# Optimization experiments

Hardware: AMD Instinct MI355X
Metric: run time of the kernel (lower is better)

The kernel has to match this reference:

```python
import jax, jax.numpy as jnp
import numpy as np

N = 131072
CODE_DIM = 64
HIDDEN = 128
DT_MAX = 0.125
N_STEPS = 8  # = ceil(max|t1-t2| / DT_MAX); extra steps are exact no-ops since dt=0 for finished rows


def setup_inputs() -> dict:
    key = jax.random.key(0)
    ks = jax.random.split(key, 8)
    deform_code = jax.random.normal(ks[0], (N, CODE_DIM), dtype=jnp.float32)
    pos_init = jax.random.normal(ks[1], (N, 3), dtype=jnp.float32)
    t1 = jax.random.uniform(ks[2], (N, 1), dtype=jnp.float32)
    t2 = jnp.zeros((N, 1), dtype=jnp.float32)
    # vel_net MLP params: concat(code, xyzt)[68] -> 128 -> 128 -> 3, tanh activations
    s1 = 1.0 / np.sqrt(CODE_DIM + 4)
    s2 = 1.0 / np.sqrt(HIDDEN)
    W1 = jax.random.normal(ks[3], (CODE_DIM + 4, HIDDEN), dtype=jnp.float32) * s1
    b1 = jnp.zeros((HIDDEN,), dtype=jnp.float32)
    W2 = jax.random.normal(ks[4], (HIDDEN, HIDDEN), dtype=jnp.float32) * s2
    b2 = jnp.zeros((HIDDEN,), dtype=jnp.float32)
    W3 = jax.random.normal(ks[5], (HIDDEN, 3), dtype=jnp.float32) * s2
    b3 = jnp.zeros((3,), dtype=jnp.float32)
    return {"deform_code": deform_code, "pos_init": pos_init, "t1": t1, "t2": t2,
            "W1": W1, "b1": b1, "W2": W2, "b2": b2, "W3": W3, "b3": b3}


def reference(deform_code, pos_init, t1, t2, W1, b1, W2, b2, W3, b3):
    def get_vel(code, xyzt):  # works for single sample or batch
        x = jnp.concatenate([code, xyzt], axis=-1)
        h = jnp.tanh(x @ W1 + b1)
        h = jnp.tanh(h @ W2 + b2)
        return h @ W3 + b3

    def u_func(code, xyzt):  # per-sample, for jacobian wrt xyzt (argnums=1)
        u = get_vel(code, xyzt)
        return u, u

    jac_fn = jax.vmap(jax.jacrev(u_func, argnums=1, has_aux=True))  # [N,3,4] jac, [N,3] vel

    n = pos_init.shape[0]
    deform0 = jnp.broadcast_to(jnp.eye(3, dtype=pos_init.dtype), (n, 3, 3))

    def step(state, _):
        xyz, t_curr, offset, deform = state
        # dt == 0 exactly for finished rows -> all updates below are no-ops (matches masked in-place updates)
        dt = jnp.sign(offset) * jnp.minimum(jnp.abs(offset), DT_MAX)  # [N,1]
        v0 = get_vel(deform_code, jnp.concatenate([xyz, t_curr], axis=-1))
        p_mid = xyz - 0.5 * dt * v0
        t_mid = t_curr - 0.5 * dt
        jac_v, velocity = jac_fn(deform_code, jnp.concatenate([p_mid, t_mid], axis=-1))
        drotdt = jnp.einsum('noi,nij->noj', jac_v[:, :3, :3], deform)
        deform = deform - dt[..., None] * drotdt
        xyz = xyz - dt * velocity
        return (xyz, t_curr - dt, offset - dt, deform), None

    state0 = (pos_init, t1, t1 - t2, deform0)
    (xyz, _, _, deform), _ = jax.lax.scan(step, state0, None, length=N_STEPS)
    return xyz, deform
```

## Files before the change

kernel.cpp:

```cpp
#include <hip/hip_runtime.h>
#include <hip/hip_bf16.h>

#define H 128
#define NSTEPS 8
#define DT_MAXF 0.125f
#define WAVES 4
#define PPW 16
#define PPB (WAVES*PPW)

typedef __attribute__((ext_vector_type(8))) short short8;
typedef __attribute__((ext_vector_type(4))) float floatx4;
typedef __attribute__((ext_vector_type(2))) float f32x2;

__device__ __forceinline__ f32x2 sp2(float v) { return (f32x2){v, v}; }
__device__ __forceinline__ f32x2 fma2(f32x2 a, f32x2 b, f32x2 c) {
    return __builtin_elementwise_fma(a, b, c);
}
__device__ __forceinline__ f32x2 tanh2(f32x2 x) {
    f32x2 y = x * 2.8853900817779268f;
    f32x2 e; e[0] = __builtin_amdgcn_exp2f(y[0]); e[1] = __builtin_amdgcn_exp2f(y[1]);
    f32x2 ep = e + 1.0f;
    float rt = __builtin_amdgcn_rcpf(ep[0] * ep[1]);
    f32x2 eps = __builtin_shufflevector(ep, ep, 1, 0);
    f32x2 r = eps * sp2(rt);
    return fma2(sp2(-2.0f), r, sp2(1.0f));
}
__device__ __forceinline__ unsigned f2bf(float x) {
    unsigned u = __float_as_uint(x);
    return (u + 0x7FFFu + ((u >> 16) & 1u)) >> 16;
}
__device__ __forceinline__ unsigned pk2(float a, float b) {
    union { __hip_bfloat162 h; unsigned u; } U;
    U.h = __float22bfloat162_rn(make_float2(a, b));
    return U.u;
}
__device__ __forceinline__ unsigned pkv(f32x2 v) { return pk2(v[0], v[1]); }
__device__ __forceinline__ short8 mk8(unsigned a, unsigned b, unsigned c, unsigned d) {
    union { unsigned u[4]; short8 s; } U;
    U.u[0] = a; U.u[1] = b; U.u[2] = c; U.u[3] = d; return U.s;
}
__device__ __forceinline__ short8 xyzt_frag(float x, float y, float z, float t, int q) {
    unsigned hx = f2bf(x), hy = f2bf(y), hz = f2bf(z), ht = f2bf(t);
    float lx = x - __uint_as_float(hx << 16);
    float ly = y - __uint_as_float(hy << 16);
    float lz = z - __uint_as_float(hz << 16);
    float lt = t - __uint_as_float(ht << 16);
    unsigned w0 = hx | (hy << 16), w1 = hz | (ht << 16);
    unsigned w2 = pk2(lx, ly),     w3 = pk2(lz, lt);
    union { unsigned u[4]; short8 s; } F;
    F.u[0] = (q < 2)  ? w0 : 0u;
    F.u[1] = (q < 2)  ? w1 : 0u;
    F.u[2] = (q == 0) ? w2 : 0u;
    F.u[3] = (q == 0) ? w3 : 0u;
    return F.s;
}

__device__ __forceinline__ int step_bucket(float t1v, float t2v) {
    float off = fabsf(t1v - t2v);
    int b = (int)ceilf(off * 8.0f);
    return min(max(b, 0), 8);
}
__global__ void prep_zero(unsigned* cnt) {
    if (threadIdx.x < 18) cnt[threadIdx.x] = 0u;
}
__global__ void prep_hist(const float* __restrict__ t1g, const float* __restrict__ t2g,
                          unsigned* cnt, int N) {
    __shared__ unsigned h[9];
    if (threadIdx.x < 9) h[threadIdx.x] = 0u;
    __syncthreads();
    int i = blockIdx.x * 256 + threadIdx.x;
    if (i < N) atomicAdd(&h[step_bucket(t1g[i], t2g[i])], 1u);
    __syncthreads();
    if (threadIdx.x < 9 && h[threadIdx.x]) atomicAdd(&cnt[threadIdx.x], h[threadIdx.x]);
}
__global__ void prep_prefix(unsigned* cnt) {
    if (threadIdx.x == 0) {
        unsigned run = 0;
        for (int b = 0; b < 9; ++b) { unsigned c = cnt[b]; cnt[9 + b] = run; run += c; }
    }
}
__global__ void prep_scatter(const float* __restrict__ t1g, const float* __restrict__ t2g,
                             unsigned* cnt, int* __restrict__ perm, int N) {
    __shared__ unsigned h[9];
    __shared__ unsigned base[9];
    if (threadIdx.x < 9) h[threadIdx.x] = 0u;
    __syncthreads();
    int i = blockIdx.x * 256 + threadIdx.x;
    int b = 0; unsigned r = 0;
    if (i < N) {
        b = step_bucket(t1g[i], t2g[i]);
        r = atomicAdd(&h[b], 1u);
    }
    __syncthreads();
    if (threadIdx.x < 9 && h[threadIdx.x])
        base[threadIdx.x] = atomicAdd(&cnt[9 + threadIdx.x], h[threadIdx.x]);
    __syncthreads();
    if (i < N) perm[base[b] + r] = i;
}

__global__ __launch_bounds__(256, 2)
void velwarp(const float* __restrict__ code, const float* __restrict__ pos,
             const float* __restrict__ t1g, const float* __restrict__ t2g,
             const float* __restrict__ W1, const float* __restrict__ b1,
             const float* __restrict__ W2, const float* __restrict__ b2,
             const float* __restrict__ W3, const float* __restrict__ b3,
             float* __restrict__ out, const int* __restrict__ perm, int N)
{
    __shared__ __align__(16) uint4 WbufU[2048];
    __shared__ __align__(16) uint4 W1AU[8*64];
    __shared__ __align__(16) uint4 W3AU[4*64];
    __shared__ __align__(16) floatx4 WdX4[32];
    __shared__ __align__(16) floatx4 WdY4[32];
    __shared__ __align__(16) floatx4 WdZ4[32];
    __shared__ __align__(16) floatx4 b2C4[32];

    const int tid = threadIdx.x;
    const int L   = tid & 63;
    const int m   = L & 15;
    const int q   = L >> 4;
    const int pb  = blockIdx.x * PPB + (tid >> 6) * PPW;
    const int p   = perm ? perm[pb + m] : (pb + m);

    {
        const float4* s4 = (const float4*)W1;
        float4* d4 = (float4*)WbufU;
        #pragma unroll 4
        for (int i = tid; i < (64*H)/4; i += 256) d4[i] = s4[i];
    }
    for (int e = tid; e < 512; e += 256) {
        int t = e >> 6, l = e & 63;
        int u = t*16 + (l & 15), qq = l >> 4;
        unsigned hb[4], lb[4];
        #pragma unroll
        for (int c = 0; c < 4; ++c) {
            float wv = W1[(64 + c)*H + u];
            unsigned hh = f2bf(wv);
            float wl = wv - __uint_as_float(hh << 16);
            hb[c] = hh; lb[c] = f2bf(wl);
        }
        unsigned hi01 = hb[0] | (hb[1] << 16), hi23 = hb[2] | (hb[3] << 16);
        unsigned lo01 = lb[0] | (lb[1] << 16), lo23 = lb[2] | (lb[3] << 16);
        uint4 o;
        if (qq == 0)      o = make_uint4(hi01, hi23, hi01, hi23);
        else if (qq == 1) o = make_uint4(lo01, lo23, 0u, 0u);
        else              o = make_uint4(0u, 0u, 0u, 0u);
        W1AU[e] = o;
    }
    for (int e = tid; e < 256; e += 256) {
        int s = e >> 6, l = e & 63;
        int a = l & 15, qq = l >> 4;
        uint4 o = make_uint4(0u, 0u, 0u, 0u);
        if (a < 3) {
            int u0 = s*32 + qq*4, u1 = u0 + 16;
            o.x = f2bf(W3[(u0+0)*3+a]) | (f2bf(W3[(u0+1)*3+a]) << 16);
            o.y = f2bf(W3[(u0+2)*3+a]) | (f2bf(W3[(u0+3)*3+a]) << 16);
            o.z = f2bf(W3[(u1+0)*3+a]) | (f2bf(W3[(u1+1)*3+a]) << 16);
            o.w = f2bf(W3[(u1+2)*3+a]) | (f2bf(W3[(u1+3)*3+a]) << 16);
        }
        W3AU[e] = o;
    }
    if (tid < 32) {
        WdX4[tid] = ((const floatx4*)(W1 + (size_t)64*H))[tid];
        WdY4[tid] = ((const floatx4*)(W1 + (size_t)65*H))[tid];
        WdZ4[tid] = ((const floatx4*)(W1 + (size_t)66*H))[tid];
        b2C4[tid] = ((const floatx4*)b2)[tid];
    }
    __syncthreads();

    floatx4 base1C[8];
    {
        #pragma unroll
        for (int t = 0; t < 8; ++t) base1C[t] = *(const floatx4*)&b1[t*16 + q*4];
        const float* Ws = (const float*)WbufU;
        const float* crow = code + (size_t)p * 64;
        for (int i = 0; i < 64; ++i) {
            f32x2 c = sp2(crow[i]);
            #pragma unroll
            for (int t = 0; t < 8; ++t) {
                floatx4 wq = *(const floatx4*)&Ws[i*H + t*16 + q*4];
                base1C[t].xy = fma2(c, wq.xy, base1C[t].xy);
                base1C[t].zw = fma2(c, wq.zw, base1C[t].zw);
            }
        }
    }
    __syncthreads();

    for (int ch = tid; ch < 2048; ch += 256) {
        int ln = ch & 63, ts = ch >> 6;
        int s = ts & 3, t = ts >> 2;
        int qq = ln >> 4, n = t*16 + (ln & 15);
        int u0 = s*32 + qq*4, u1 = u0 + 16;
        unsigned w0 = f2bf(W2[(u0+0)*H+n]) | (f2bf(W2[(u0+1)*H+n]) << 16);
        unsigned w1 = f2bf(W2[(u0+2)*H+n]) | (f2bf(W2[(u0+3)*H+n]) << 16);
        unsigned w2 = f2bf(W2[(u1+0)*H+n]) | (f2bf(W2[(u1+1)*H+n]) << 16);
        unsigned w3v = f2bf(W2[(u1+2)*H+n]) | (f2bf(W2[(u1+3)*H+n]) << 16);
        WbufU[ch] = make_uint4(w0, w1, w2, w3v);
    }

    float px_ = pos[p*3+0], py_ = pos[p*3+1], pz_ = pos[p*3+2];
    float tc_ = t1g[p];
    float off_ = tc_ - t2g[p];
    f32x2 Dp[3]; float Ds[3];
    Dp[0] = (f32x2){1.f, 0.f}; Ds[0] = 0.f;
    Dp[1] = (f32x2){0.f, 1.f}; Ds[1] = 0.f;
    Dp[2] = (f32x2){0.f, 0.f}; Ds[2] = 1.f;
    const float b30 = b3[0], b31 = b3[1], b32 = b3[2];
    __syncthreads();

    const short8* Bf   = (const short8*)WbufU;
    const short8* W1Af = (const short8*)W1AU;
    const short8* W3Af = (const short8*)W3AU;
    const floatx4 Z4 = {0.f, 0.f, 0.f, 0.f};

    for (int step = 0; step < NSTEPS; ++step) {
        if (!__any(off_ != 0.0f)) break;

        float vAx, vAy, vAz;
        {
            short8 xf = xyzt_frag(px_, py_, pz_, tc_, q);
            floatx4 z[8];
            #pragma unroll
            for (int t = 0; t < 8; ++t)
                z[t] = __builtin_amdgcn_mfma_f32_16x16x32_bf16(W1Af[t*64 + L], xf, base1C[t], 0, 0, 0);
            short8 fh[4];
            #pragma unroll
            for (int s = 0; s < 4; ++s) {
                f32x2 a0 = tanh2(z[2*s].xy),   a1 = tanh2(z[2*s].zw);
                f32x2 c0 = tanh2(z[2*s+1].xy), c1 = tanh2(z[2*s+1].zw);
                fh[s] = mk8(pkv(a0), pkv(a1), pkv(c0), pkv(c1));
            }
            __builtin_amdgcn_sched_barrier(0);
            floatx4 vacc = Z4;
            #pragma unroll
            for (int qi = 0; qi < 4; ++qi) {
                const int T0 = 2*qi, T1 = 2*qi + 1;
                floatx4 acc0 = __builtin_amdgcn_mfma_f32_16x16x32_bf16(
                    Bf[(T0*4 + 0)*64 + L], fh[0], b2C4[T0*4 + q], 0, 0, 0);
                floatx4 acc1 = __builtin_amdgcn_mfma_f32_16x16x32_bf16(
                    Bf[(T1*4 + 0)*64 + L], fh[0], b2C4[T1*4 + q], 0, 0, 0);
                #pragma unroll
                for (int s = 1; s < 4; ++s) {
                    acc0 = __builtin_amdgcn_mfma_f32_16x16x32_bf16(Bf[(T0*4 + s)*64 + L], fh[s], acc0, 0, 0, 0);
                    acc1 = __builtin_amdgcn_mfma_f32_16x16x32_bf16(Bf[(T1*4 + s)*64 + L], fh[s], acc1, 0, 0, 0);
                }
                f32x2 e00 = tanh2(acc0.xy), e01 = tanh2(acc0.zw);
                f32x2 e10 = tanh2(acc1.xy), e11 = tanh2(acc1.zw);
                short8 ef = mk8(pkv(e00), pkv(e01), pkv(e10), pkv(e11));
                vacc = __builtin_amdgcn_mfma_f32_16x16x32_bf16(W3Af[qi*64 + L], ef, vacc, 0, 0, 0);
                __builtin_amdgcn_sched_barrier(0);
            }
            vAx = __shfl(vacc[0], m, 64);
            vAy = __shfl(vacc[1], m, 64);
            vAz = __shfl(vacc[2], m, 64);
        }

        float dt_ = copysignf(fminf(fabsf(off_), DT_MAXF), off_);
        float hd = 0.5f * dt_;
        float mx = px_ - hd*(vAx + b30);
        float my = py_ - hd*(vAy + b31);
        float mz = pz_ - hd*(vAz + b32);
        float tm = tc_ - hd;

        float vx, vy, vz;
        floatx4 V = Z4, J0 = Z4, J1 = Z4, J2 = Z4;
        {
            short8 xf = xyzt_frag(mx, my, mz, tm, q);
            floatx4 z[8];
            #pragma unroll
            for (int t = 0; t < 8; ++t)
                z[t] = __builtin_amdgcn_mfma_f32_16x16x32_bf16(W1Af[t*64 + L], xf, base1C[t], 0, 0, 0);
            short8 fh[4], fd0[4], fd1[4], fd2[4];
            #pragma unroll
            for (int s = 0; s < 4; ++s) {
                unsigned uh[4], u0[4], u1[4], u2[4];
                #pragma unroll
                for (int hf = 0; hf < 2; ++hf) {
                    int t = 2*s + hf;
                    f32x2 h0 = tanh2(z[t].xy), h1 = tanh2(z[t].zw);
                    f32x2 s0 = fma2(-h0, h0, sp2(1.0f));
                    f32x2 s1 = fma2(-h1, h1, sp2(1.0f));
                    floatx4 wx = WdX4[t*4 + q], wy = WdY4[t*4 + q], wz = WdZ4[t*4 + q];
                    uh[2*hf+0] = pkv(h0);         uh[2*hf+1] = pkv(h1);
                    u0[2*hf+0] = pkv(s0 * wx.xy); u0[2*hf+1] = pkv(s1 * wx.zw);
                    u1[2*hf+0] = pkv(s0 * wy.xy); u1[2*hf+1] = pkv(s1 * wy.zw);
                    u2[2*hf+0] = pkv(s0 * wz.xy); u2[2*hf+1] = pkv(s1 * wz.zw);
                }
                fh[s]  = mk8(uh[0], uh[1], uh[2], uh[3]);
                fd0[s] = mk8(u0[0], u0[1], u0[2], u0[3]);
                fd1[s] = mk8(u1[0], u1[1], u1[2], u1[3]);
                fd2[s] = mk8(u2[0], u2[1], u2[2], u2[3]);
            }
            __builtin_amdgcn_sched_barrier(0);
            #pragma unroll
            for (int qi = 0; qi < 4; ++qi) {
                const int T0 = 2*qi, T1 = 2*qi + 1;
                floatx4 aH0, aH1, aD00, aD01, aD10, aD11, aD20, aD21;
                {
                    short8 A0 = Bf[(T0*4 + 0)*64 + L];
                    short8 A1 = Bf[(T1*4 + 0)*64 + L];
                    aH0  = __builtin_amdgcn_mfma_f32_16x16x32_bf16(A0, fh[0],  b2C4[T0*4 + q], 0, 0, 0);
                    aH1  = __builtin_amdgcn_mfma_f32_16x16x32_bf16(A1, fh[0],  b2C4[T1*4 + q], 0, 0, 0);
                    aD00 = __builtin_amdgcn_mfma_f32_16x16x32_bf16(A0, fd0[0], Z4, 0, 0, 0);
                    aD01 = __builtin_amdgcn_mfma_f32_16x16x32_bf16(A1, fd0[0], Z4, 0, 0, 0);
                    aD10 = __builtin_amdgcn_mfma_f32_16x16x32_bf16(A0, fd1[0], Z4, 0, 0, 0);
                    aD11 = __builtin_amdgcn_mfma_f32_16x16x32_bf16(A1, fd1[0], Z4, 0, 0, 0);
                    aD20 = __builtin_amdgcn_mfma_f32_16x16x32_bf16(A0, fd2[0], Z4, 0, 0, 0);
                    aD21 = __builtin_amdgcn_mfma_f32_16x16x32_bf16(A1, fd2[0], Z4, 0, 0, 0);
                }
                #pragma unroll
                for (int s = 1; s < 4; ++s) {
                    short8 A0 = Bf[(T0*4 + s)*64 + L];
                    short8 A1 = Bf[(T1*4 + s)*64 + L];
                    aH0  = __builtin_amdgcn_mfma_f32_16x16x32_bf16(A0, fh[s],  aH0,  0, 0, 0);
                    aH1  = __builtin_amdgcn_mfma_f32_16x16x32_bf16(A1, fh[s],  aH1,  0, 0, 0);
                    aD00 = __builtin_amdgcn_mfma_f32_16x16x32_bf16(A0, fd0[s], aD00, 0, 0, 0);
                    aD01 = __builtin_amdgcn_mfma_f32_16x16x32_bf16(A1, fd0[s], aD01, 0, 0, 0);
                    aD10 = __builtin_amdgcn_mfma_f32_16x16x32_bf16(A0, fd1[s], aD10, 0, 0, 0);
                    aD11 = __builtin_amdgcn_mfma_f32_16x16x32_bf16(A1, fd1[s], aD11, 0, 0, 0);
                    aD20 = __builtin_amdgcn_mfma_f32_16x16x32_bf16(A0, fd2[s], aD20, 0, 0, 0);
                    aD21 = __builtin_amdgcn_mfma_f32_16x16x32_bf16(A1, fd2[s], aD21, 0, 0, 0);
                }
                f32x2 h0 = tanh2(aH0.xy), h1 = tanh2(aH0.zw);
                f32x2 h2v = tanh2(aH1.xy), h3 = tanh2(aH1.zw);
                f32x2 s0 = fma2(-h0, h0, sp2(1.0f));
                f32x2 s1 = fma2(-h1, h1, sp2(1.0f));
                f32x2 s2v = fma2(-h2v, h2v, sp2(1.0f));
                f32x2 s3 = fma2(-h3, h3, sp2(1.0f));
                short8 eh = mk8(pkv(h0), pkv(h1), pkv(h2v), pkv(h3));
                short8 e0 = mk8(pkv(s0*aD00.xy), pkv(s1*aD00.zw), pkv(s2v*aD01.xy), pkv(s3*aD01.zw));
                short8 e1 = mk8(pkv(s0*aD10.xy), pkv(s1*aD10.zw), pkv(s2v*aD11.xy), pkv(s3*aD11.zw));
                short8 e2 = mk8(pkv(s0*aD20.xy), pkv(s1*aD20.zw), pkv(s2v*aD21.xy), pkv(s3*aD21.zw));
                const short8 WA = W3Af[qi*64 + L];
                V  = __builtin_amdgcn_mfma_f32_16x16x32_bf16(WA, eh, V,  0, 0, 0);
                J0 = __builtin_amdgcn_mfma_f32_16x16x32_bf16(WA, e0, J0, 0, 0, 0);
                J1 = __builtin_amdgcn_mfma_f32_16x16x32_bf16(WA, e1, J1, 0, 0, 0);
                J2 = __builtin_amdgcn_mfma_f32_16x16x32_bf16(WA, e2, J2, 0, 0, 0);
                __builtin_amdgcn_sched_barrier(0);
            }
            vx = __shfl(V[0], m, 64) + b30;
            vy = __shfl(V[1], m, 64) + b31;
            vz = __shfl(V[2], m, 64) + b32;
        }

        {
            f32x2 ndp[3]; float nds[3];
            #pragma unroll
            for (int o = 0; o < 3; ++o) {
                f32x2 tp = J0[o] * Dp[0];
                tp = fma2(sp2(J1[o]), Dp[1], tp);
                tp = fma2(sp2(J2[o]), Dp[2], tp);
                ndp[o] = fma2(sp2(-dt_), tp, Dp[o]);
                float ts = J0[o]*Ds[0];
                ts = fmaf(J1[o], Ds[1], ts);
                ts = fmaf(J2[o], Ds[2], ts);
                nds[o] = fmaf(-dt_, ts, Ds[o]);
            }
            #pragma unroll
            for (int o = 0; o < 3; ++o) { Dp[o] = ndp[o]; Ds[o] = nds[o]; }
        }
        px_ = fmaf(-dt_, vx, px_);
        py_ = fmaf(-dt_, vy, py_);
        pz_ = fmaf(-dt_, vz, pz_);
        tc_  -= dt_;
        off_ -= dt_;
    }

    if (q == 0) {
        out[p*3+0] = px_; out[p*3+1] = py_; out[p*3+2] = pz_;
        float* o9 = out + (size_t)N*3 + (size_t)p*9;
        #pragma unroll
        for (int o = 0; o < 3; ++o) {
            o9[o*3+0] = Dp[o][0];
            o9[o*3+1] = Dp[o][1];
            o9[o*3+2] = Ds[o];
        }
    }
}

extern "C" void kernel_launch(void* const* d_in, const int* in_sizes, int n_in,
                              void* d_out, int out_size, void* d_ws, size_t ws_size,
                              hipStream_t stream) {
    const float* code = (const float*)d_in[0];
    const float* pos  = (const float*)d_in[1];
    const float* t1   = (const float*)d_in[2];
    const float* t2   = (const float*)d_in[3];
    const float* W1   = (const float*)d_in[4];
    const float* b1   = (const float*)d_in[5];
    const float* W2   = (const float*)d_in[6];
    const float* b2   = (const float*)d_in[7];
    const float* W3   = (const float*)d_in[8];
    const float* b3   = (const float*)d_in[9];
    float* out = (float*)d_out;
    const int N = in_sizes[1] / 3;
    const int blocks = N / PPB;

    const size_t need = 128 + (size_t)N * sizeof(int);
    int* perm = nullptr;
    if (d_ws && ws_size >= need) {
        unsigned* cnt = (unsigned*)d_ws;
        perm = (int*)((char*)d_ws + 128);
        const int pblocks = (N + 255) / 256;
        prep_zero<<<1, 64, 0, stream>>>(cnt);
        prep_hist<<<pblocks, 256, 0, stream>>>(t1, t2, cnt, N);
        prep_prefix<<<1, 64, 0, stream>>>(cnt);
        prep_scatter<<<pblocks, 256, 0, stream>>>(t1, t2, cnt, perm, N);
    }
    velwarp<<<blocks, 256, 0, stream>>>(code, pos, t1, t2, W1, b1, W2, b2, W3, b3, out, perm, N);
}
```

Before: 302.3 us.

## Compute code projection with split-bf16 MFMA, reverse bucket order, memset counters

```diff
diff --git a/kernel.cpp b/kernel.cpp
--- a/kernel.cpp
+++ b/kernel.cpp
@@ -60,9 +60,6 @@
     int b = (int)ceilf(off * 8.0f);
     return min(max(b, 0), 8);
 }
-__global__ void prep_zero(unsigned* cnt) {
-    if (threadIdx.x < 18) cnt[threadIdx.x] = 0u;
-}
 __global__ void prep_hist(const float* __restrict__ t1g, const float* __restrict__ t2g,
                           unsigned* cnt, int N) {
     __shared__ unsigned h[9];
@@ -76,7 +73,7 @@
 __global__ void prep_prefix(unsigned* cnt) {
     if (threadIdx.x == 0) {
         unsigned run = 0;
-        for (int b = 0; b < 9; ++b) { unsigned c = cnt[b]; cnt[9 + b] = run; run += c; }
+        for (int b = 8; b >= 0; --b) { unsigned c = cnt[b]; cnt[9 + b] = run; run += c; }
     }
 }
 __global__ void prep_scatter(const float* __restrict__ t1g, const float* __restrict__ t2g,
@@ -121,11 +118,24 @@
     const int pb  = blockIdx.x * PPB + (tid >> 6) * PPW;
     const int p   = perm ? perm[pb + m] : (pb + m);
 
-    {
-        const float4* s4 = (const float4*)W1;
-        float4* d4 = (float4*)WbufU;
-        #pragma unroll 4
-        for (int i = tid; i < (64*H)/4; i += 256) d4[i] = s4[i];
+    for (int e = tid; e < 1024; e += 256) {
+        int t = e >> 7, rem = e & 127;
+        int c = rem >> 6, l = rem & 63;
+        int qq = l >> 4, mm = l & 15;
+        int u = t*16 + mm;
+        int g0 = c*32 + qq*4, g1 = g0 + 16;
+        unsigned hh[8]; float lo[8];
+        #pragma unroll
+        for (int j = 0; j < 4; ++j) {
+            float w0 = W1[(g0+j)*H + u];
+            float w1 = W1[(g1+j)*H + u];
+            hh[j]   = f2bf(w0); lo[j]   = w0 - __uint_as_float(hh[j]   << 16);
+            hh[4+j] = f2bf(w1); lo[4+j] = w1 - __uint_as_float(hh[4+j] << 16);
+        }
+        WbufU[((t*2+c)*2+0)*64 + l] = make_uint4(hh[0]|(hh[1]<<16), hh[2]|(hh[3]<<16),
+                                                 hh[4]|(hh[5]<<16), hh[6]|(hh[7]<<16));
+        WbufU[((t*2+c)*2+1)*64 + l] = make_uint4(pk2(lo[0],lo[1]), pk2(lo[2],lo[3]),
+                                                 pk2(lo[4],lo[5]), pk2(lo[6],lo[7]));
     }
     for (int e = tid; e < 512; e += 256) {
         int t = e >> 6, l = e & 63;
@@ -169,18 +179,36 @@
 
     floatx4 base1C[8];
     {
+        const float4* crow4 = (const float4*)(code + (size_t)p * 64);
+        short8 Bh[2], Bl[2];
         #pragma unroll
-        for (int t = 0; t < 8; ++t) base1C[t] = *(const floatx4*)&b1[t*16 + q*4];
-        const float* Ws = (const float*)WbufU;
-        const float* crow = code + (size_t)p * 64;
-        for (int i = 0; i < 64; ++i) {
-            f32x2 c = sp2(crow[i]);
-            #pragma unroll
-            for (int t = 0; t < 8; ++t) {
-                floatx4 wq = *(const floatx4*)&Ws[i*H + t*16 + q*4];
-                base1C[t].xy = fma2(c, wq.xy, base1C[t].xy);
-                base1C[t].zw = fma2(c, wq.zw, base1C[t].zw);
-            }
+        for (int c = 0; c < 2; ++c) {
+            float4 a = crow4[c*8 + q];
+            float4 b = crow4[c*8 + 4 + q];
+            unsigned h0 = f2bf(a.x), h1 = f2bf(a.y), h2 = f2bf(a.z), h3 = f2bf(a.w);
+            unsigned g0 = f2bf(b.x), g1 = f2bf(b.y), g2 = f2bf(b.z), g3 = f2bf(b.w);
+            float l0 = a.x - __uint_as_float(h0<<16), l1 = a.y - __uint_as_float(h1<<16);
+            float l2 = a.z - __uint_as_float(h2<<16), l3 = a.w - __uint_as_float(h3<<16);
+            float m0 = b.x - __uint_as_float(g0<<16), m1 = b.y - __uint_as_float(g1<<16);
+            float m2 = b.z - __uint_as_float(g2<<16), m3 = b.w - __uint_as_float(g3<<16);
+            Bh[c] = mk8(h0|(h1<<16), h2|(h3<<16), g0|(g1<<16), g2|(g3<<16));
+            Bl[c] = mk8(pk2(l0,l1), pk2(l2,l3), pk2(m0,m1), pk2(m2,m3));
+        }
+        const short8* Wb = (const short8*)WbufU;
+        #pragma unroll
+        for (int t = 0; t < 8; ++t) {
+            floatx4 z = *(const floatx4*)&b1[t*16 + q*4];
+            short8 Wh0 = Wb[((t*2+0)*2+0)*64 + L];
+            short8 Wh1 = Wb[((t*2+1)*2+0)*64 + L];
+            short8 Wl0 = Wb[((t*2+0)*2+1)*64 + L];
+            short8 Wl1 = Wb[((t*2+1)*2+1)*64 + L];
+            z = __builtin_amdgcn_mfma_f32_16x16x32_bf16(Wh0, Bh[0], z, 0, 0, 0);
+            z = __builtin_amdgcn_mfma_f32_16x16x32_bf16(Wh1, Bh[1], z, 0, 0, 0);
+            z = __builtin_amdgcn_mfma_f32_16x16x32_bf16(Wh0, Bl[0], z, 0, 0, 0);
+            z = __builtin_amdgcn_mfma_f32_16x16x32_bf16(Wh1, Bl[1], z, 0, 0, 0);
+            z = __builtin_amdgcn_mfma_f32_16x16x32_bf16(Wl0, Bh[0], z, 0, 0, 0);
+            z = __builtin_amdgcn_mfma_f32_16x16x32_bf16(Wl1, Bh[1], z, 0, 0, 0);
+            base1C[t] = z;
         }
     }
     __syncthreads();
@@ -400,7 +428,7 @@
         unsigned* cnt = (unsigned*)d_ws;
         perm = (int*)((char*)d_ws + 128);
         const int pblocks = (N + 255) / 256;
-        prep_zero<<<1, 64, 0, stream>>>(cnt);
+        hipMemsetAsync(d_ws, 0, 128, stream);
         prep_hist<<<pblocks, 256, 0, stream>>>(t1, t2, cnt, N);
         prep_prefix<<<1, 64, 0, stream>>>(cnt);
         prep_scatter<<<pblocks, 256, 0, stream>>>(t1, t2, cnt, perm, N);
```

Result: faster. 279.0 us (-7.7%).
